# Performance work log

Hardware: AMD Instinct MI355X
Metric: run time of the kernel (lower is better)

## Reference

```python
import jax, jax.numpy as jnp
import numpy as np

GRID = 256      # spatial grid (periodic, pseudo-spectral)
BATCH = 8
N_STEPS = 4     # dynamics steps between outputs (layer arg N)
N_OUTPUT = 4    # number of outputs (layer arg n_output)
CH = 32         # Q_network hidden channels
DT = 0.01       # timestep
R_DRAG = 0.05   # linear (Ekman) drag
BETA = 0.5      # beta-plane coefficient
Q_SCALE = 0.01  # Q_callback scaling of network output
IN_W = 1.0      # input_weight
OUT_W = 1.0     # output_weight


def _wavenumbers():
    k = jnp.fft.fftfreq(GRID, 1.0 / GRID).astype(jnp.float32)  # integer wavenumbers
    KX = k[None, :]   # x varies along axis 1
    KY = k[:, None]   # y varies along axis 0
    K2 = KX * KX + KY * KY
    inv_lap = jnp.where(K2 > 0, -1.0 / jnp.where(K2 > 0, K2, 1.0), 0.0)  # psi_hat = -zeta_hat/k^2
    return KX, KY, inv_lap


def _q_network(z, W1, b1, W2, b2):
    # 2-layer 3x3 CNN forcing network on a single [H, W] field.
    x = z[None, :, :, None]  # NHWC
    dn = ('NHWC', 'HWIO', 'NHWC')
    h = jax.lax.conv_general_dilated(x, W1, (1, 1), 'SAME', dimension_numbers=dn) + b1
    h = jax.nn.relu(h)
    q = jax.lax.conv_general_dilated(h, W2, (1, 1), 'SAME', dimension_numbers=dn) + b2
    return q[0, :, :, 0]


def setup_inputs() -> dict:
    key = jax.random.key(0)
    k0, k1, k2, k3 = jax.random.split(key, 4)
    zeta = jax.random.normal(k0, (BATCH, GRID, GRID), dtype=jnp.float32)
    Q_0 = 0.1 * jax.random.normal(k1, (GRID, GRID), dtype=jnp.float32)
    W1 = 0.1 * jax.random.normal(k2, (3, 3, 1, CH), dtype=jnp.float32)
    b1 = jnp.zeros((CH,), dtype=jnp.float32)
    W2 = 0.1 * jax.random.normal(k3, (3, 3, CH, 1), dtype=jnp.float32)
    b2 = jnp.zeros((1,), dtype=jnp.float32)
    return {"zeta": zeta, "Q_0": Q_0, "W1": W1, "b1": b1, "W2": W2, "b2": b2}


def reference(zeta, Q_0, W1, b1, W2, b2):
    KX, KY, inv_lap = _wavenumbers()

    @jax.checkpoint
    def step(_, z):
        # Q_0 + Q_callback(dynamics, Q_network), evaluated before each step
        Q = Q_0 + Q_SCALE * _q_network(z, W1, b1, W2, b2)
        zh = jnp.fft.fft2(z)
        ph = zh * inv_lap                                  # solve nabla^2 psi = zeta
        u = jnp.real(jnp.fft.ifft2(-1j * KY * ph))         # u = -dpsi/dy
        v = jnp.real(jnp.fft.ifft2(1j * KX * ph))          # v =  dpsi/dx
        zx = jnp.real(jnp.fft.ifft2(1j * KX * zh))
        zy = jnp.real(jnp.fft.ifft2(1j * KY * zh))
        adv = u * zx + v * zy
        return z + DT * (-adv - BETA * v - R_DRAG * z + Q)

    def compute_step_outputs(z, _):
        z = jax.lax.fori_loop(0, N_STEPS, step, z)
        return z, z * OUT_W

    def compute_outputs(z0):
        _, outs = jax.lax.scan(compute_step_outputs, z0 * IN_W, None, length=N_OUTPUT)
        return outs  # [n_output, H, W]

    return jax.vmap(compute_outputs)(zeta)  # [batch, n_output, H, W]
```

## Files before the change

kernel.cpp:

```cpp
#include <hip/hip_runtime.h>

#define NG 256
#define PI2F 6.28318530717958647692f
#define PIDX(i) ((i) + ((i) >> 4))
#define HT_CELL 36

__device__ __forceinline__ float2 f2add(float2 a, float2 b){ return make_float2(a.x+b.x, a.y+b.y); }
__device__ __forceinline__ float2 f2sub(float2 a, float2 b){ return make_float2(a.x-b.x, a.y-b.y); }
__device__ __forceinline__ float2 cmul(float2 a, float2 b){ return make_float2(a.x*b.x - a.y*b.y, a.x*b.y + a.y*b.x); }

template<bool INV>
__device__ __forceinline__ void fft256_r4(float2* a, float2* b, const float2* tw,
                                          int u, bool act)
{
#pragma unroll
    for (int st = 0; st < 4; ++st) {
        if (act) {
            const int sl = 2 * st;
            const int q  = u & ((1 << sl) - 1);
            const int j1 = u - q;
            const float2 x0 = a[PIDX(u)];
            const float2 x1 = a[PIDX(u + 64)];
            const float2 x2 = a[PIDX(u + 128)];
            const float2 x3 = a[PIDX(u + 192)];
            float2 w1 = tw[j1];
            if (INV) w1.y = -w1.y;
            const float2 w2 = cmul(w1, w1);
            const float2 w3 = cmul(w1, w2);
            const float2 apc = f2add(x0, x2), amc = f2sub(x0, x2);
            const float2 bpd = f2add(x1, x3), bmd = f2sub(x1, x3);
            const float2 jb  = make_float2(-bmd.y, bmd.x);
            const float2 t0  = f2add(apc, bpd);
            const float2 t2  = f2sub(apc, bpd);
            const float2 t1  = INV ? f2add(amc, jb) : f2sub(amc, jb);
            const float2 t3  = INV ? f2sub(amc, jb) : f2add(amc, jb);
            const int wb = q + (j1 << 2);
            const int ss = 1 << sl;
            b[PIDX(wb)]          = t0;
            b[PIDX(wb + ss)]     = cmul(w1, t1);
            b[PIDX(wb + 2 * ss)] = cmul(w2, t2);
            b[PIDX(wb + 3 * ss)] = cmul(w3, t3);
        }
        __syncthreads();
        float2* tmp = a; a = b; b = tmp;
    }
}

__device__ __forceinline__ void init_tw(float2* tw, int tid)
{
    if (tid < 256) {
        float s, c;
        __sincosf(-PI2F * (float)tid * (1.f / 256.f), &s, &c);
        tw[tid] = make_float2(c, s);
    }
}

#define R_POOL 19456

__global__ void __launch_bounds__(256)
r_kernel(const float* zin, float* zout,
         const float2* __restrict__ Ct0, const float2* __restrict__ Ct1,
         float2* __restrict__ At, const float* __restrict__ Qb,
         float* __restrict__ outp, int do_d, int do_a)
{
    __shared__ __align__(16) char pool[R_POOL];
    float2* tw   = (float2*)pool;
    float2* bufs = (float2*)(pool + 2048);
    const int tid = threadIdx.x;
    const int b   = blockIdx.x >> 7;
    const int y0  = (blockIdx.x & 127) * 2;
    const int j   = tid >> 6, u = tid & 63;

    init_tw(tw, tid);

    if (do_d) {
        float2* A = bufs + j * 272;
        float2* B = bufs + (4 + j) * 272;
        const float2* src = ((j & 1) ? Ct1 : Ct0)
                          + ((size_t)(b * NG + y0 + (j >> 1))) * NG;
#pragma unroll
        for (int r4 = 0; r4 < 4; ++r4) {
            const int x = u + 64 * r4;
            A[PIDX(x)] = src[x];
        }
        __syncthreads();
        fft256_r4<true>(A, B, tw, u, true);

        const float sc = 1.f / 256.f;
        float zn01[2];
#pragma unroll
        for (int r = 0; r < 2; ++r) {
            const float2 uvv = (bufs + (2 * r) * 272)[PIDX(tid)];
            const float2 gzz = (bufs + (2 * r + 1) * 272)[PIDX(tid)];
            const float uu = uvv.x * sc, vv = uvv.y * sc;
            const float zx = gzz.x * sc, zy = gzz.y * sc;
            const int idx = (b * NG + y0 + r) * NG + tid;
            const float z0v = zin[idx];
            const float qv  = Qb[idx];
            const float adv = uu * zx + vv * zy;
            const float zn = z0v + 0.01f * (-adv - 0.5f * vv - 0.05f * z0v + qv);
            zout[idx] = zn;
            if (outp) outp[b * (4 * NG * NG) + (y0 + r) * NG + tid] = zn;
            zn01[r] = zn;
        }
        __syncthreads();
        bufs[PIDX(tid)] = make_float2(zn01[0], zn01[1]);
        __syncthreads();
    } else {
        bufs[PIDX(tid)] = make_float2(zin[(b * NG + y0) * NG + tid],
                                      zin[(b * NG + y0 + 1) * NG + tid]);
        __syncthreads();
    }

    if (do_a) {
        fft256_r4<false>(bufs, bufs + 4 * 272, tw, u, j == 0);
        const int k  = tid;
        const int km = (256 - k) & 255;
        const float2 Zk = bufs[PIDX(k)], Zm = bufs[PIDX(km)];
        const float dx = Zk.x - Zm.x, dy = Zk.y + Zm.y;
        const float4 ov = make_float4(0.5f * (Zk.x + Zm.x), 0.5f * (Zk.y - Zm.y),
                                      0.5f * dy, -0.5f * dx);
        *((float4*)(At + ((size_t)(b * NG + k)) * NG + y0)) = ov;
    }
}

#define COL_POOL 50704

__global__ void __launch_bounds__(512)
col_kernel(const float2* __restrict__ At, float2* __restrict__ Ct0,
           float2* __restrict__ Ct1, const float* __restrict__ zsrc,
           const float* __restrict__ Q0, const float* __restrict__ W1,
           const float* __restrict__ b1, const float* __restrict__ W2,
           const float* __restrict__ b2, float* __restrict__ Qb)
{
    __shared__ __align__(16) char pool[COL_POOL];
    const int tid = threadIdx.x;

    if (blockIdx.x < 2048) {
        float*  zt  = (float*)pool;
        float*  ht  = (float*)(pool + 1600);
        float4* w1s = (float4*)(pool + 48256);
        float4* w2s = (float4*)(pool + 49408);
        float*  b1s = (float*)(pool + 50560);
        float*  b2s = (float*)(pool + 50688);
        const int b   = blockIdx.x >> 8;
        const int ty0 = ((blockIdx.x >> 4) & 15) * 16, tx0 = (blockIdx.x & 15) * 16;

        if (tid < 72) {
            w1s[tid] = ((const float4*)W1)[tid];
            w2s[tid] = ((const float4*)W2)[tid];
        }
        if (tid < 32) b1s[tid] = b1[tid];
        if (tid == 0) b2s[0] = b2[0];

        for (int i = tid; i < 400; i += 512) {
            const int ly = i / 20, lx = i - ly * 20;
            const int gy = ty0 + ly - 2, gx = tx0 + lx - 2;
            float v = 0.f;
            if ((unsigned)gy < 256u && (unsigned)gx < 256u)
                v = zsrc[(b * NG + gy) * NG + gx];
            zt[ly * 20 + lx] = v;
        }
        __syncthreads();

        for (int i = tid; i < 324 * 8; i += 512) {
            const int pos = i >> 3, cg = i & 7;
            const int hy = pos / 18, hx = pos - hy * 18;
            const int gy = ty0 + hy - 1, gx = tx0 + hx - 1;
            float4 acc = make_float4(0.f, 0.f, 0.f, 0.f);
            if ((unsigned)gy < 256u && (unsigned)gx < 256u) {
                acc = make_float4(b1s[cg * 4], b1s[cg * 4 + 1],
                                  b1s[cg * 4 + 2], b1s[cg * 4 + 3]);
#pragma unroll
                for (int dy = 0; dy < 3; dy++)
#pragma unroll
                    for (int dx = 0; dx < 3; dx++) {
                        const float zv = zt[(hy + dy) * 20 + hx + dx];
                        const float4 w = w1s[(dy * 3 + dx) * 8 + cg];
                        acc.x += w.x * zv; acc.y += w.y * zv;
                        acc.z += w.z * zv; acc.w += w.w * zv;
                    }
                acc.x = fmaxf(acc.x, 0.f); acc.y = fmaxf(acc.y, 0.f);
                acc.z = fmaxf(acc.z, 0.f); acc.w = fmaxf(acc.w, 0.f);
            }
            *((float4*)&ht[pos * HT_CELL + cg * 4]) = acc;
        }
        __syncthreads();

        const int px = tid >> 1, half = tid & 1;
        const int oy = px >> 4, ox = px & 15;
        float qv = half ? 0.f : b2s[0];
#pragma unroll
        for (int dy = 0; dy < 3; dy++)
#pragma unroll
            for (int dx = 0; dx < 3; dx++) {
                const float* hc = &ht[((oy + dy) * 18 + (ox + dx)) * HT_CELL + half * 16];
#pragma unroll
                for (int cg2 = 0; cg2 < 4; cg2++) {
                    const float4 hv = *((const float4*)(hc + cg2 * 4));
                    const float4 w  = w2s[(dy * 3 + dx) * 8 + half * 4 + cg2];
                    qv += w.x * hv.x + w.y * hv.y + w.z * hv.z + w.w * hv.w;
                }
            }
        qv += __shfl_xor(qv, 1);
        if (!half) {
            const int gy = ty0 + oy, gx = tx0 + ox;
            Qb[(b * NG + gy) * NG + gx] = Q0[gy * NG + gx] + 0.01f * qv;
        }
    } else {
        float2* tw   = (float2*)pool;
        float2* bufs = (float2*)(pool + 2048);
        const int bid = blockIdx.x - 2048;
        const int b  = bid >> 6;
        const int kg = bid & 63;
        const int j8 = tid >> 6, u = tid & 63;

        init_tw(tw, tid);
        if (j8 < 4) {
            const int kxl = 4 * kg + j8;
            float2* A = bufs + j8 * 272;
            const float2* src = At + ((size_t)(b * NG + kxl)) * NG;
#pragma unroll
            for (int r = 0; r < 4; ++r) {
                const int x = u + 64 * r;
                A[PIDX(x)] = src[x];
            }
        }
        __syncthreads();
        fft256_r4<false>(bufs + j8 * 272, bufs + (4 + (j8 & 3)) * 272, tw, u, j8 < 4);

        if (tid < 256) {
            const int jl = tid >> 6;
            const int kxl = 4 * kg + jl;
            float2* A = bufs + jl * 272;
            float2* C = bufs + (8 + jl) * 272;
            const float kxv = (kxl < 128) ? (float)kxl : (float)(kxl - 256);
            const float kxm = (kxl == 128) ? 0.f : kxv;
#pragma unroll
            for (int r = 0; r < 4; ++r) {
                const int ky = u + 64 * r;
                const float kyv = (ky < 128) ? (float)ky : (float)(ky - 256);
                const float kym = (ky == 128) ? 0.f : kyv;
                const float K2 = kxv * kxv + kyv * kyv;
                const float il = (K2 > 0.f) ? (-1.f / K2) : 0.f;
                const float2 Z = A[PIDX(ky)];
                const float ar = -kxm * il, ai = -kym * il;
                A[PIDX(ky)] = make_float2(ar * Z.x - ai * Z.y, ar * Z.y + ai * Z.x);
                C[PIDX(ky)] = make_float2(-kym * Z.x - kxm * Z.y, -kym * Z.y + kxm * Z.x);
            }
        }
        __syncthreads();

        float2* ia = (j8 < 4) ? bufs + j8 * 272 : bufs + (8 + (j8 - 4)) * 272;
        float2* ib = (j8 < 4) ? bufs + (4 + j8) * 272 : bufs + (12 + (j8 - 4)) * 272;
        fft256_r4<true>(ia, ib, tw, u, true);

        const float sc = 1.f / 256.f;
        const int y = tid & 255;
        float2 ov[4];
        if (tid < 256) {
#pragma unroll
            for (int jj = 0; jj < 4; ++jj) {
                const float2 r0 = (bufs + jj * 272)[PIDX(y)];
                ov[jj] = make_float2(r0.x * sc, r0.y * sc);
            }
            float4* dst = (float4*)(Ct0 + ((size_t)(b * NG + y)) * NG + 4 * kg);
            dst[0] = ((float4*)ov)[0];
            dst[1] = ((float4*)ov)[1];
        } else {
#pragma unroll
            for (int jj = 0; jj < 4; ++jj) {
                const float2 r1 = (bufs + (8 + jj) * 272)[PIDX(y)];
                ov[jj] = make_float2(r1.x * sc, r1.y * sc);
            }
            float4* dst = (float4*)(Ct1 + ((size_t)(b * NG + y)) * NG + 4 * kg);
            dst[0] = ((float4*)ov)[0];
            dst[1] = ((float4*)ov)[1];
        }
    }
}

extern "C" void kernel_launch(void* const* d_in, const int* in_sizes, int n_in,
                              void* d_out, int out_size, void* d_ws, size_t ws_size,
                              hipStream_t stream)
{
    const float* zeta = (const float*)d_in[0];
    const float* Q0   = (const float*)d_in[1];
    const float* W1   = (const float*)d_in[2];
    const float* b1   = (const float*)d_in[3];
    const float* W2   = (const float*)d_in[4];
    const float* b2   = (const float*)d_in[5];
    float* outp = (float*)d_out;

    char* ws = (char*)d_ws;
    float*  zws = (float*)(ws);
    float*  Qb  = (float*)(ws + (2u << 20));
    float2* At  = (float2*)(ws + (4u << 20));
    float2* Ct0 = (float2*)(ws + (8u << 20));
    float2* Ct1 = (float2*)(ws + (12u << 20));
    if (ws_size < (16u << 20)) return;

    r_kernel<<<1024, 256, 0, stream>>>(zeta, zws, Ct0, Ct1, At, Qb,
                                       nullptr, 0, 1);
    for (int j = 1; j <= 16; ++j) {
        const float* zp = (j == 1) ? zeta : zws;
        col_kernel<<<2560, 512, 0, stream>>>(At, Ct0, Ct1, zp,
                                             Q0, W1, b1, W2, b2, Qb);
        float* op = (j % 4 == 0) ? (outp + (size_t)(j / 4 - 1) * NG * NG)
                                 : nullptr;
        r_kernel<<<1024, 256, 0, stream>>>(zp, zws, Ct0, Ct1, At, Qb,
                                           op, 1, (j < 16) ? 1 : 0);
    }
}
```

Measured before the change: 666.5 us.

## Register-block the Q-network conv layers with vectorized loads and swizzled hidden tile

The two 3x3 conv layers of the forcing network are restructured. Each thread now computes four horizontal outputs for eight channels from float4 loads of a widened input tile. The hidden activations are stored with a per-cell channel-group swizzle so the second conv can read them without bank conflicts. The second conv has each thread produce four outputs and reduce across channel groups with shuffles, then write the result as a float4. Launch bounds now request 6 blocks per SM, which trades register headroom for occupancy and could cause spills in the FFT branch sharing the kernel.

```diff
diff --git a/kernel.cpp b/kernel.cpp
--- a/kernel.cpp
+++ b/kernel.cpp
@@ -3,11 +3,20 @@
 #define NG 256
 #define PI2F 6.28318530717958647692f
 #define PIDX(i) ((i) + ((i) >> 4))
-#define HT_CELL 36
 
 __device__ __forceinline__ float2 f2add(float2 a, float2 b){ return make_float2(a.x+b.x, a.y+b.y); }
 __device__ __forceinline__ float2 f2sub(float2 a, float2 b){ return make_float2(a.x-b.x, a.y-b.y); }
 __device__ __forceinline__ float2 cmul(float2 a, float2 b){ return make_float2(a.x*b.x - a.y*b.y, a.x*b.y + a.y*b.x); }
+__device__ __forceinline__ float comp(float4 v, int p) {
+    return p == 0 ? v.x : p == 1 ? v.y : p == 2 ? v.z : v.w;
+}
+__device__ __forceinline__ float4 f4fma(float4 a, float4 v, float s) {
+    return make_float4(fmaf(v.x, s, a.x), fmaf(v.y, s, a.y),
+                       fmaf(v.z, s, a.z), fmaf(v.w, s, a.w));
+}
+__device__ __forceinline__ float dot4(float4 a, float4 b) {
+    return a.x * b.x + a.y * b.y + a.z * b.z + a.w * b.w;
+}
 
 template<bool INV>
 __device__ __forceinline__ void fft256_r4(float2* a, float2* b, const float2* tw,
@@ -124,9 +133,9 @@
     }
 }
 
-#define COL_POOL 50704
-
-__global__ void __launch_bounds__(512)
+#define COL_POOL 51344
+
+__global__ void __launch_bounds__(512, 6)
 col_kernel(const float2* __restrict__ At, float2* __restrict__ Ct0,
            float2* __restrict__ Ct1, const float* __restrict__ zsrc,
            const float* __restrict__ Q0, const float* __restrict__ W1,
@@ -138,11 +147,11 @@
 
     if (blockIdx.x < 2048) {
         float*  zt  = (float*)pool;
-        float*  ht  = (float*)(pool + 1600);
-        float4* w1s = (float4*)(pool + 48256);
-        float4* w2s = (float4*)(pool + 49408);
-        float*  b1s = (float*)(pool + 50560);
-        float*  b2s = (float*)(pool + 50688);
+        float*  ht  = (float*)(pool + 2240);
+        float4* w1s = (float4*)(pool + 48896);
+        float4* w2s = (float4*)(pool + 50048);
+        float*  b1s = (float*)(pool + 51200);
+        float*  b2s = (float*)(pool + 51328);
         const int b   = blockIdx.x >> 8;
         const int ty0 = ((blockIdx.x >> 4) & 15) * 16, tx0 = (blockIdx.x & 15) * 16;
 
@@ -153,59 +162,113 @@
         if (tid < 32) b1s[tid] = b1[tid];
         if (tid == 0) b2s[0] = b2[0];
 
-        for (int i = tid; i < 400; i += 512) {
-            const int ly = i / 20, lx = i - ly * 20;
-            const int gy = ty0 + ly - 2, gx = tx0 + lx - 2;
-            float v = 0.f;
+        for (int i = tid; i < 120; i += 512) {
+            const int r = i / 6, c4 = i - r * 6;
+            const int gy = ty0 - 2 + r;
+            const int gx = tx0 - 4 + 4 * c4;
+            float4 v = make_float4(0.f, 0.f, 0.f, 0.f);
             if ((unsigned)gy < 256u && (unsigned)gx < 256u)
-                v = zsrc[(b * NG + gy) * NG + gx];
-            zt[ly * 20 + lx] = v;
-        }
-        __syncthreads();
-
-        for (int i = tid; i < 324 * 8; i += 512) {
-            const int pos = i >> 3, cg = i & 7;
-            const int hy = pos / 18, hx = pos - hy * 18;
-            const int gy = ty0 + hy - 1, gx = tx0 + hx - 1;
-            float4 acc = make_float4(0.f, 0.f, 0.f, 0.f);
-            if ((unsigned)gy < 256u && (unsigned)gx < 256u) {
-                acc = make_float4(b1s[cg * 4], b1s[cg * 4 + 1],
-                                  b1s[cg * 4 + 2], b1s[cg * 4 + 3]);
-#pragma unroll
-                for (int dy = 0; dy < 3; dy++)
-#pragma unroll
-                    for (int dx = 0; dx < 3; dx++) {
-                        const float zv = zt[(hy + dy) * 20 + hx + dx];
-                        const float4 w = w1s[(dy * 3 + dx) * 8 + cg];
-                        acc.x += w.x * zv; acc.y += w.y * zv;
-                        acc.z += w.z * zv; acc.w += w.w * zv;
+                v = *((const float4*)&zsrc[(b * NG + gy) * NG + gx]);
+            *((float4*)&zt[r * 28 + 4 * c4]) = v;
+        }
+        __syncthreads();
+
+        if (tid < 360) {
+            const int chunk = tid >> 2, cgp = tid & 3;
+            const int hy = chunk / 5, hx0 = (chunk - hy * 5) * 4;
+            const int k4 = hx0;
+            float4 hacc[8];
+#pragma unroll
+            for (int c = 0; c < 8; ++c) {
+                const float bv = b1s[cgp * 8 + c];
+                hacc[c] = make_float4(bv, bv, bv, bv);
+            }
+#pragma unroll
+            for (int dy = 0; dy < 3; ++dy) {
+                const float* zrow = &zt[(hy + dy) * 28 + k4];
+                const float4 Az = *((const float4*)zrow);
+                const float4 Bz = *((const float4*)(zrow + 4));
+                const float4 W0 = make_float4(Az.z, Az.w, Bz.x, Bz.y);
+                const float4 W1v = make_float4(Az.w, Bz.x, Bz.y, Bz.z);
+#pragma unroll
+                for (int g = 0; g < 2; ++g) {
+                    const float4 wa = w1s[(dy * 3 + 0) * 8 + 2 * cgp + g];
+                    const float4 wb = w1s[(dy * 3 + 1) * 8 + 2 * cgp + g];
+                    const float4 wc = w1s[(dy * 3 + 2) * 8 + 2 * cgp + g];
+                    hacc[4*g+0] = f4fma(f4fma(f4fma(hacc[4*g+0], W0, wa.x), W1v, wb.x), Bz, wc.x);
+                    hacc[4*g+1] = f4fma(f4fma(f4fma(hacc[4*g+1], W0, wa.y), W1v, wb.y), Bz, wc.y);
+                    hacc[4*g+2] = f4fma(f4fma(f4fma(hacc[4*g+2], W0, wa.z), W1v, wb.z), Bz, wc.z);
+                    hacc[4*g+3] = f4fma(f4fma(f4fma(hacc[4*g+3], W0, wa.w), W1v, wb.w), Bz, wc.w);
+                }
+            }
+            const int gyh = ty0 - 1 + hy;
+            const bool vy = (unsigned)gyh < 256u;
+#pragma unroll
+            for (int p = 0; p < 4; ++p) {
+                const int hxc = hx0 + p;
+                if (hxc < 18) {
+                    const float mk = (vy && (unsigned)(tx0 - 1 + hxc) < 256u) ? 1.f : 0.f;
+                    float* cellp = &ht[(hy * 18 + hxc) * 36];
+                    const int s0 = ((2 * cgp + 0 + hxc) & 7) << 2;
+                    const int s1 = ((2 * cgp + 1 + hxc) & 7) << 2;
+                    const float4 lo = make_float4(
+                        mk * fmaxf(comp(hacc[0], p), 0.f), mk * fmaxf(comp(hacc[1], p), 0.f),
+                        mk * fmaxf(comp(hacc[2], p), 0.f), mk * fmaxf(comp(hacc[3], p), 0.f));
+                    const float4 hi = make_float4(
+                        mk * fmaxf(comp(hacc[4], p), 0.f), mk * fmaxf(comp(hacc[5], p), 0.f),
+                        mk * fmaxf(comp(hacc[6], p), 0.f), mk * fmaxf(comp(hacc[7], p), 0.f));
+                    *((float4*)(cellp + s0)) = lo;
+                    *((float4*)(cellp + s1)) = hi;
+                }
+            }
+        }
+        __syncthreads();
+
+        {
+            const int chunk = tid >> 3, cg = tid & 7;
+            const int oy = chunk >> 2, ox4 = (chunk & 3) * 4;
+            float q0 = 0.f, q1 = 0.f, q2 = 0.f, q3 = 0.f;
+#pragma unroll
+            for (int dy = 0; dy < 3; ++dy) {
+                const float* hrow = &ht[((oy + dy) * 18 + ox4) * 36];
+                const float4 wA = w2s[(dy * 3 + 0) * 8 + cg];
+                const float4 wB = w2s[(dy * 3 + 1) * 8 + cg];
+                const float4 wC = w2s[(dy * 3 + 2) * 8 + cg];
+#pragma unroll
+                for (int jj = 0; jj < 6; ++jj) {
+                    const float4 hv = *((const float4*)(hrow + jj * 36
+                                        + (((cg + ox4 + jj) & 7) << 2)));
+                    if (jj <= 3) {
+                        const float d = dot4(hv, wA);
+                        if (jj == 0) q0 += d; else if (jj == 1) q1 += d;
+                        else if (jj == 2) q2 += d; else q3 += d;
                     }
-                acc.x = fmaxf(acc.x, 0.f); acc.y = fmaxf(acc.y, 0.f);
-                acc.z = fmaxf(acc.z, 0.f); acc.w = fmaxf(acc.w, 0.f);
-            }
-            *((float4*)&ht[pos * HT_CELL + cg * 4]) = acc;
-        }
-        __syncthreads();
-
-        const int px = tid >> 1, half = tid & 1;
-        const int oy = px >> 4, ox = px & 15;
-        float qv = half ? 0.f : b2s[0];
-#pragma unroll
-        for (int dy = 0; dy < 3; dy++)
-#pragma unroll
-            for (int dx = 0; dx < 3; dx++) {
-                const float* hc = &ht[((oy + dy) * 18 + (ox + dx)) * HT_CELL + half * 16];
-#pragma unroll
-                for (int cg2 = 0; cg2 < 4; cg2++) {
-                    const float4 hv = *((const float4*)(hc + cg2 * 4));
-                    const float4 w  = w2s[(dy * 3 + dx) * 8 + half * 4 + cg2];
-                    qv += w.x * hv.x + w.y * hv.y + w.z * hv.z + w.w * hv.w;
+                    if (jj >= 1 && jj <= 4) {
+                        const float d = dot4(hv, wB);
+                        if (jj == 1) q0 += d; else if (jj == 2) q1 += d;
+                        else if (jj == 3) q2 += d; else q3 += d;
+                    }
+                    if (jj >= 2) {
+                        const float d = dot4(hv, wC);
+                        if (jj == 2) q0 += d; else if (jj == 3) q1 += d;
+                        else if (jj == 4) q2 += d; else q3 += d;
+                    }
                 }
             }
-        qv += __shfl_xor(qv, 1);
-        if (!half) {
-            const int gy = ty0 + oy, gx = tx0 + ox;
-            Qb[(b * NG + gy) * NG + gx] = Q0[gy * NG + gx] + 0.01f * qv;
+#pragma unroll
+            for (int s = 1; s < 8; s <<= 1) {
+                q0 += __shfl_xor(q0, s); q1 += __shfl_xor(q1, s);
+                q2 += __shfl_xor(q2, s); q3 += __shfl_xor(q3, s);
+            }
+            if (cg == 0) {
+                const int gy = ty0 + oy, gx = tx0 + ox4;
+                const float4 Qv = *((const float4*)&Q0[gy * NG + gx]);
+                const float bb = b2s[0];
+                const float4 o = make_float4(
+                    Qv.x + 0.01f * (q0 + bb), Qv.y + 0.01f * (q1 + bb),
+                    Qv.z + 0.01f * (q2 + bb), Qv.w + 0.01f * (q3 + bb));
+                *((float4*)&Qb[(b * NG + gy) * NG + gx]) = o;
+            }
         }
     } else {
         float2* tw   = (float2*)pool;
```

Result: slower. 1.502 ms (+125.3%).
